# Performance work log

Measured on AMD Instinct MI355X. Metric: run time of the kernel, lower is better.

Reference implementation:

```python
import jax, jax.numpy as jnp
import numpy as np


def setup_inputs() -> dict:
    key = jax.random.key(0)
    k1, k2, k3 = jax.random.split(key, 3)
    x1 = jax.random.normal(k1, (6, 3, 256, 256), dtype=jnp.float32)
    # ConvTranspose2d(3,3,1) weight layout in torch is (in_ch, out_ch, 1, 1); squeeze to (in, out)
    W = jax.random.normal(k2, (3, 3), dtype=jnp.float32) * 0.3
    b = jax.random.normal(k3, (3,), dtype=jnp.float32) * 0.1
    return {"x1": x1, "W": W, "b": b}


def reference(x1, W, b):
    # 1x1 transposed conv == per-pixel channel mix: y[b,o,h,w] = sum_i x[b,i,h,w] * W[i,o] + b[o]
    v1 = jnp.einsum('bihw,io->bohw', x1, W) + b[None, :, None, None]
    v2 = v1 + 3.0
    v3 = v2 * 3.0
    v4 = jax.nn.relu(v3)
    v5 = v4 + 3.0
    v6 = jax.nn.relu(v5)
    v7 = v6 * 3.0
    v8 = v7 + 3.0
    v10 = jnp.tile(v6, (1, 3, 1, 1))           # [B,9,H,W]
    v11 = jnp.tile(v2, (1, 3, 1, 1))           # [B,9,H,W]
    v12 = jnp.transpose(v11, (0, 1, 3, 2))     # [B,9,W,H]
    v13 = jnp.transpose(v10, (0, 2, 1, 3))     # [B,H,9,W]
    v14 = v7 - 3.0
    v15 = jax.nn.relu(v14)
    v16 = v15 - 3.0
    v17 = jax.nn.relu(v16)
    v18 = v17 - 3.0
    v19 = jax.nn.relu(v18)
    v20 = v19 - 3.0
    v21 = v20 - 3.0
    v24 = jnp.tile(v12, (1, 1, 1, 3))          # [B,9,W,3H]
    v25 = jnp.tile(v13, (1, 1, 1, 3))          # [B,H,9,3W]
    v26 = jnp.transpose(v24, (0, 3, 1, 2))     # [B,3H,9,W]
    v28 = jnp.transpose(v25, (0, 3, 1, 2))     # [B,3W,H,9]
    v30 = jnp.tile(v26, (1, 1, 1, 3))          # [B,3H,9,3W]
    v33 = jnp.tile(v28, (1, 1, 1, 3))          # [B,3W,H,27]
    v37 = jnp.tile(v30, (2, 1, 1, 1))          # [2B,3H,9,3W]
    v42 = jnp.split(v24, 3, axis=0)            # chunk(3) along batch
    v43 = jnp.split(v25, 3, axis=0)
    v46 = jnp.concatenate(v42, axis=1)         # [B/3,27,W,3H]
    v47 = jnp.concatenate(v43, axis=3)         # [B/3,H,9,9W]
    m1 = jnp.max(v37, axis=0)                  # [3H,9,3W] = [768,9,768]
    out = (m1 + jnp.max(v46) + jnp.min(v47) + jnp.max(v8)
           + jnp.min(v21) + jnp.min(v33))
    return out
```

## Files before the change

### kernel.cpp

```cpp
#include <hip/hip_runtime.h>

static constexpr int NPIX = 256 * 256;

typedef float f4 __attribute__((ext_vector_type(4)));

__device__ __forceinline__ float chain_v6(float v2) {
    return fmaxf(fmaxf(3.0f * v2, 0.0f) + 3.0f, 0.0f);
}
__device__ __forceinline__ float chain_v21(float v2) {
    float t = 3.0f * chain_v6(v2);
    t = fmaxf(t - 3.0f, 0.0f);
    t = fmaxf(t - 3.0f, 0.0f);
    t = fmaxf(t - 3.0f, 0.0f);
    return t - 6.0f;
}

__global__ __launch_bounds__(256) void k_compute(const float* __restrict__ x,
                                                 const float* __restrict__ Wp,
                                                 const float* __restrict__ bp,
                                                 float* __restrict__ M,
                                                 float2* __restrict__ partials) {
    const int t = threadIdx.x;
    const int p = blockIdx.x * 256 + t;
    const int lane = t & 63, wid = t >> 6;

    float W[9];
#pragma unroll
    for (int i = 0; i < 9; ++i) W[i] = Wp[i];
    const float bias[3] = {bp[0], bp[1], bp[2]};

    float Mc[3] = {-3.4e38f, -3.4e38f, -3.4e38f};
    float minv2 = 3.4e38f;

#pragma unroll
    for (int b = 0; b < 6; ++b) {
        const float x0 = x[(b * 3 + 0) * NPIX + p];
        const float x1 = x[(b * 3 + 1) * NPIX + p];
        const float x2 = x[(b * 3 + 2) * NPIX + p];
#pragma unroll
        for (int c = 0; c < 3; ++c) {
            float v2 = fmaf(x0, W[c], fmaf(x1, W[3 + c], fmaf(x2, W[6 + c], bias[c] + 3.0f)));
            Mc[c] = fmaxf(Mc[c], v2);
            minv2 = fminf(minv2, v2);
        }
    }

    M[0 * NPIX + p] = Mc[0];
    M[1 * NPIX + p] = Mc[1];
    M[2 * NPIX + p] = Mc[2];

    float maxv2 = fmaxf(Mc[0], fmaxf(Mc[1], Mc[2]));
#pragma unroll
    for (int o = 32; o > 0; o >>= 1) {
        maxv2 = fmaxf(maxv2, __shfl_down(maxv2, o));
        minv2 = fminf(minv2, __shfl_down(minv2, o));
    }
    __shared__ float smx[4], smn[4];
    if (lane == 0) { smx[wid] = maxv2; smn[wid] = minv2; }
    __syncthreads();
    if (t == 0) {
        partials[blockIdx.x] =
            make_float2(fmaxf(fmaxf(smx[0], smx[1]), fmaxf(smx[2], smx[3])),
                        fminf(fminf(smn[0], smn[1]), fminf(smn[2], smn[3])));
    }
}

__global__ __launch_bounds__(256) void k_out(const f4* __restrict__ Mv,
                                             const float2* __restrict__ partials,
                                             f4* __restrict__ out) {
    const int t = threadIdx.x;
    const int lane = t & 63, wid = t >> 6;

    float2 pr = partials[t];
    float A = pr.x, B = pr.y;
#pragma unroll
    for (int o = 32; o > 0; o >>= 1) {
        A = fmaxf(A, __shfl_down(A, o));
        B = fminf(B, __shfl_down(B, o));
    }
    __shared__ float sA[4], sB[4];
    if (lane == 0) { sA[wid] = A; sB[wid] = B; }
    __syncthreads();
    const float Ag = fmaxf(fmaxf(sA[0], sA[1]), fmaxf(sA[2], sA[3]));
    const float Bg = fminf(fminf(sB[0], sB[1]), fminf(sB[2], sB[3]));
    const float S = Ag + 2.0f * chain_v6(Bg) + (3.0f * chain_v6(Ag) + 3.0f) + chain_v21(Bg);

    const int jbase = blockIdx.x * 2048 + t;
#pragma unroll
    for (int i = 0; i < 8; ++i) {
        const int j = jbase + i * 256;
        const int row = j / 192;
        const int w4 = j - row * 192;
        const int c = row % 3;
        const int xr = (row / 9) & 255;
        f4 m = Mv[c * (NPIX / 4) + xr * 64 + (w4 & 63)];
        __builtin_nontemporal_store(m + S, &out[j]);
    }
}

extern "C" void kernel_launch(void* const* d_in, const int* in_sizes, int n_in,
                              void* d_out, int out_size, void* d_ws, size_t ws_size,
                              hipStream_t stream) {
    const float* x = (const float*)d_in[0];
    const float* W = (const float*)d_in[1];
    const float* b = (const float*)d_in[2];

    float* M = (float*)d_ws;
    float2* partials = (float2*)((char*)d_ws + 3 * NPIX * 4);

    hipLaunchKernelGGL(k_compute, dim3(NPIX / 256), dim3(256), 0, stream, x, W, b, M, partials);
    hipLaunchKernelGGL(k_out, dim3(648), dim3(256), 0, stream, (const f4*)M, partials, (f4*)d_out);
}
```

Measured before the change: 15.32 us.

## Reorganize output kernel grid to load each M row once and store three replicas

The output kernel now uses a 2D grid of (channel, output row) with 192 threads per block. Each thread loads one float4 of M once and writes it to the three replicated positions along the row, which removes the per-element div/mod index arithmetic and cuts redundant M reads. The partials reduction is adjusted for 192 threads, and input loads in the compute kernel become nontemporal. The cost is many more, smaller blocks (2304 blocks of 192 threads), each repeating the 256-partial reduction.

```diff
diff --git a/kernel.cpp b/kernel.cpp
--- a/kernel.cpp
+++ b/kernel.cpp
@@ -34,9 +34,9 @@
 
 #pragma unroll
     for (int b = 0; b < 6; ++b) {
-        const float x0 = x[(b * 3 + 0) * NPIX + p];
-        const float x1 = x[(b * 3 + 1) * NPIX + p];
-        const float x2 = x[(b * 3 + 2) * NPIX + p];
+        const float x0 = __builtin_nontemporal_load(&x[(b * 3 + 0) * NPIX + p]);
+        const float x1 = __builtin_nontemporal_load(&x[(b * 3 + 1) * NPIX + p]);
+        const float x2 = __builtin_nontemporal_load(&x[(b * 3 + 2) * NPIX + p]);
 #pragma unroll
         for (int c = 0; c < 3; ++c) {
             float v2 = fmaf(x0, W[c], fmaf(x1, W[3 + c], fmaf(x2, W[6 + c], bias[c] + 3.0f)));
@@ -65,7 +65,7 @@
     }
 }
 
-__global__ __launch_bounds__(256) void k_out(const f4* __restrict__ Mv,
+__global__ __launch_bounds__(192) void k_out(const f4* __restrict__ Mv,
                                              const float2* __restrict__ partials,
                                              f4* __restrict__ out) {
     const int t = threadIdx.x;
@@ -73,29 +73,32 @@
 
     float2 pr = partials[t];
     float A = pr.x, B = pr.y;
+    if (t < 64) {
+        float2 q = partials[192 + t];
+        A = fmaxf(A, q.x);
+        B = fminf(B, q.y);
+    }
 #pragma unroll
     for (int o = 32; o > 0; o >>= 1) {
         A = fmaxf(A, __shfl_down(A, o));
         B = fminf(B, __shfl_down(B, o));
     }
-    __shared__ float sA[4], sB[4];
+    __shared__ float sA[3], sB[3];
     if (lane == 0) { sA[wid] = A; sB[wid] = B; }
     __syncthreads();
-    const float Ag = fmaxf(fmaxf(sA[0], sA[1]), fmaxf(sA[2], sA[3]));
-    const float Bg = fminf(fminf(sB[0], sB[1]), fminf(sB[2], sB[3]));
+    const float Ag = fmaxf(sA[0], fmaxf(sA[1], sA[2]));
+    const float Bg = fminf(sB[0], fminf(sB[1], sB[2]));
     const float S = Ag + 2.0f * chain_v6(Bg) + (3.0f * chain_v6(Ag) + 3.0f) + chain_v21(Bg);
 
-    const int jbase = blockIdx.x * 2048 + t;
-#pragma unroll
-    for (int i = 0; i < 8; ++i) {
-        const int j = jbase + i * 256;
-        const int row = j / 192;
-        const int w4 = j - row * 192;
-        const int c = row % 3;
-        const int xr = (row / 9) & 255;
-        f4 m = Mv[c * (NPIX / 4) + xr * 64 + (w4 & 63)];
-        __builtin_nontemporal_store(m + S, &out[j]);
-    }
+    const int c = blockIdx.x;
+    const int xr = blockIdx.y;
+
+    const f4 m = Mv[c * (NPIX / 4) + (xr & 255) * 64 + (t & 63)];
+    const f4 r = m + S;
+    const int base = (xr * 9 + c) * 192 + t;
+    __builtin_nontemporal_store(r, &out[base]);
+    __builtin_nontemporal_store(r, &out[base + 576]);
+    __builtin_nontemporal_store(r, &out[base + 1152]);
 }
 
 extern "C" void kernel_launch(void* const* d_in, const int* in_sizes, int n_in,
@@ -109,5 +112,5 @@
     float2* partials = (float2*)((char*)d_ws + 3 * NPIX * 4);
 
     hipLaunchKernelGGL(k_compute, dim3(NPIX / 256), dim3(256), 0, stream, x, W, b, M, partials);
-    hipLaunchKernelGGL(k_out, dim3(648), dim3(256), 0, stream, (const f4*)M, partials, (f4*)d_out);
+    hipLaunchKernelGGL(k_out, dim3(3, 768), dim3(192), 0, stream, (const f4*)M, partials, (f4*)d_out);
 }
```

New measurement: 15.08 us. About the same (-1.6%).
